# Kernel optimization log

Hardware: AMD Instinct MI355X
Metric: run time of the kernel (lower is better)

Reference implementation:

```python
import jax, jax.numpy as jnp
import numpy as np

FRAC_BIT = 12
SCALE = float(2 ** FRAC_BIT)          # 12 fractional bits
QMIN, QMAX = -32768.0, 32767.0        # signed 16-bit two's complement range


def quant16(x):
    """Quantize to signed 16-bit fixed point with 12 fractional bits.

    Matches float_to_16bits_tensor / bit_slice semantics: the bit-serial
    crossbar MVM of the sliced operands equals an exact integer product of
    these fixed-point values, rescaled back to float.
    """
    return jnp.clip(jnp.round(x * SCALE), QMIN, QMAX) / SCALE


def setup_inputs() -> dict:
    key = jax.random.key(0)
    k1, k2 = jax.random.split(key)
    x = jax.random.normal(k1, (32, 128, 56, 56), dtype=jnp.float32)
    # kaiming-ish scale so weights are well inside the fixed-point range
    weight = jax.random.normal(k2, (256, 128, 3, 3), dtype=jnp.float32) * 0.05
    return {"x": x, "weight": weight}


def reference(x, weight):
    # The nested i/j loop in the original slides a stride-1 window over the
    # zero-padded input, performing a bit-sliced crossbar MVM per pixel.
    # That is exactly conv2d(stride=1, padding=1) on 16-bit fixed-point
    # quantized input and weight (bias row in the crossbar is zero / unused).
    qx = quant16(x)
    qw = quant16(weight)
    out = jax.lax.conv_general_dilated(
        qx, qw,
        window_strides=(1, 1),
        padding=((1, 1), (1, 1)),
        dimension_numbers=("NCHW", "OIHW", "NCHW"),
    )
    return out
```

## Files before the change

### kernel.cpp

```cpp
#include <hip/hip_runtime.h>
#include <cstdint>
#include <cstddef>


typedef __attribute__((ext_vector_type(8))) short short8;
typedef __attribute__((ext_vector_type(4))) float floatx4;

#define NIMG 32
#define CIN  128
#define HW   56
#define KOUT 256
#define HP   58
#define XPAD_ELEMS ((size_t)NIMG * HP * HP * CIN)
#define WT_OFF_BYTES (XPAD_ELEMS * 2)
#define KK 1152

__device__ __forceinline__ uint16_t quant_bf16(float v) {
    float q = rintf(v * 4096.0f);
    q = fminf(fmaxf(q, -32768.0f), 32767.0f) * (1.0f / 4096.0f);
    union { float f; uint32_t u; } cv; cv.f = q;
    uint32_t u = cv.u;
    return (uint16_t)((u + 0x7fffu + ((u >> 16) & 1u)) >> 16);
}

__global__ __launch_bounds__(256) void quant_pad_x(const float* __restrict__ x,
                                                   uint16_t* __restrict__ xp) {
    const int b = blockIdx.x;
    const int n = b / HP, hp = b - n * HP;
    uint16_t* row = xp + (size_t)(n * HP + hp) * HP * CIN;

    if (hp == 0 || hp == HP - 1) {
        uint4 z{0, 0, 0, 0};
        uint4* d = (uint4*)row;
        for (int t = threadIdx.x; t < HP * CIN * 2 / 16; t += 256) d[t] = z;
        return;
    }
    const int h = hp - 1;
    __shared__ uint16_t tile[HW * 130];
    const float* src = x + (size_t)n * CIN * HW * HW + (size_t)h * HW;
    for (int t = threadIdx.x; t < CIN * 14; t += 256) {
        int c = t / 14, w4 = t - c * 14;
        float4 v = *(const float4*)(src + (size_t)c * (HW * HW) + w4 * 4);
        int base = (w4 * 4) * 130 + c;
        tile[base]       = quant_bf16(v.x);
        tile[base + 130] = quant_bf16(v.y);
        tile[base + 260] = quant_bf16(v.z);
        tile[base + 390] = quant_bf16(v.w);
    }
    __syncthreads();
    if (threadIdx.x < 32) {
        uint4 z{0, 0, 0, 0};
        if (threadIdx.x < 16) ((uint4*)row)[threadIdx.x] = z;
        else ((uint4*)(row + 57 * CIN))[threadIdx.x - 16] = z;
    }
    uint2* dst = (uint2*)(row + CIN);
    for (int t = threadIdx.x; t < (HW * CIN) / 4; t += 256) {
        int w = t >> 5, c4 = (t & 31) * 4;
        uint32_t a = tile[w * 130 + c4]     | ((uint32_t)tile[w * 130 + c4 + 1] << 16);
        uint32_t c = tile[w * 130 + c4 + 2] | ((uint32_t)tile[w * 130 + c4 + 3] << 16);
        dst[t] = make_uint2(a, c);
    }
}

__global__ __launch_bounds__(256) void quant_w(const float* __restrict__ w,
                                               uint16_t* __restrict__ wt) {
    int i = blockIdx.x * 256 + threadIdx.x;
    int k = i / KK;
    int r = i - k * KK;
    int tap = r >> 7;
    int c = r & 127;
    wt[i] = quant_bf16(w[(size_t)(k * CIN + c) * 9 + tap]);
}


#define GLOAD(gsrc, ldst)                                                      \
    __builtin_amdgcn_global_load_lds(                                          \
        (__attribute__((address_space(1))) void*)(void*)(gsrc),                \
        (__attribute__((address_space(3))) void*)(void*)(ldst), 16, 0, 0)

#define STAGE_A(bsel, kt) do {                                                 \
    GLOAD(aGp[0][0] + (size_t)(kt) * 64, &ldsA[bsel][0][(wv * 8) * 64]);       \
    GLOAD(aGp[0][1] + (size_t)(kt) * 64, &ldsA[bsel][0][(64 + wv * 8) * 64]);  \
    GLOAD(aGp[1][0] + (size_t)(kt) * 64, &ldsA[bsel][1][(wv * 8) * 64]);       \
    GLOAD(aGp[1][1] + (size_t)(kt) * 64, &ldsA[bsel][1][(64 + wv * 8) * 64]);  \
} while (0)

#define STAGE_B(bsel, kt) do {                                                 \
    const int tap_ = (kt) >> 1;                                                \
    const size_t boff_ = (size_t)((tap_ / 3) * HP + (tap_ % 3)) * CIN          \
                       + (size_t)((kt) & 1) * 64;                              \
    GLOAD(bGp[0][0] + boff_, &ldsB[bsel][0][(wv * 8) * 64]);                   \
    GLOAD(bGp[0][1] + boff_, &ldsB[bsel][0][(64 + wv * 8) * 64]);              \
    GLOAD(bGp[1][0] + boff_, &ldsB[bsel][1][(wv * 8) * 64]);                   \
    GLOAD(bGp[1][1] + boff_, &ldsB[bsel][1][(64 + wv * 8) * 64]);              \
} while (0)

#define READ_A(bsel, q4) do {                                                  \
    _Pragma("unroll")                                                          \
    for (int f_ = 0; f_ < 4; ++f_) {                                           \
        const int r_ = (q4) * 64 + f_ * 16 + m16;                              \
        ra[f_][0] = *(const short8*)&ldsA[bsel][wm][r_ * 64 + sl0];            \
        ra[f_][1] = *(const short8*)&ldsA[bsel][wm][r_ * 64 + sl1];            \
    }                                                                          \
} while (0)

#define READ_B(dst, bsel, ch) do {                                             \
    _Pragma("unroll")                                                          \
    for (int fc_ = 0; fc_ < 2; ++fc_) {                                        \
        const int r_ = bl + (ch) * 32 + fc_ * 16 + m16;                        \
        dst[fc_][0] = *(const short8*)&ldsB[bsel][bh][r_ * 64 + sl0];          \
        dst[fc_][1] = *(const short8*)&ldsB[bsel][bh][r_ * 64 + sl1];          \
    }                                                                          \
} while (0)

#define MFMA_Q(q4, ch, B) do {                                                 \
    _Pragma("unroll")                                                          \
    for (int s_ = 0; s_ < 2; ++s_)                                             \
    _Pragma("unroll")                                                          \
    for (int f_ = 0; f_ < 4; ++f_)                                             \
    _Pragma("unroll")                                                          \
    for (int c_ = 0; c_ < 2; ++c_)                                             \
        acc[q4][f_][ch][c_] = __builtin_amdgcn_mfma_f32_16x16x32_bf16(         \
            ra[f_][s_], B[c_][s_], acc[q4][f_][ch][c_], 0, 0, 0);              \
} while (0)

#define KT_BODY(bsel) do {                                                     \
    READ_A(bsel, 0);                                                           \
    READ_B(rb0, bsel, 0);                                                      \
    READ_B(rb1, bsel, 1);                                                      \
    __builtin_amdgcn_s_setprio(1);                                             \
    MFMA_Q(0, 0, rb0);                                                         \
    MFMA_Q(0, 1, rb1);                                                         \
    __builtin_amdgcn_s_setprio(0);                                             \
    READ_A(bsel, 1);                   \
    __builtin_amdgcn_s_setprio(1);                                             \
    MFMA_Q(1, 0, rb0);                                                         \
    MFMA_Q(1, 1, rb1);                                                         \
    __builtin_amdgcn_s_setprio(0);                                             \
} while (0)

#define KT_SYNC_STAGE(bsel, ktn) do {                                          \
    __builtin_amdgcn_s_barrier();                                              \
    STAGE_A(bsel, ktn); STAGE_B(bsel, ktn);                                    \
    asm volatile("s_waitcnt vmcnt(8)" ::: "memory");                           \
    __builtin_amdgcn_s_barrier();                                              \
} while (0)

__global__ __launch_bounds__(512, 2) void conv_gemm(const uint16_t* __restrict__ xp,
                                                    const uint16_t* __restrict__ wt,
                                                    float* __restrict__ out) {
    __shared__ __align__(16) uint16_t ldsA[2][2][128 * 64];
    __shared__ __align__(16) uint16_t ldsB[2][2][128 * 64];

    const int tid  = threadIdx.x;
    const int l    = tid & 63;
    const int wv   = tid >> 6;
    const int wm   = wv >> 2;
    const int wn   = wv & 3;
    const int bh   = wn >> 1;
    const int bl   = (wn & 1) * 64;
    const int srow = l >> 3;
    const int c_data = (l & 7) ^ srow;
    const int m16  = l & 15;
    const int q    = l >> 4;
    const int r7   = m16 & 7;
    const int sl0  = ((0 + q) ^ r7) * 8;
    const int sl1  = ((4 + q) ^ r7) * 8;

    const int b = blockIdx.x;
    const int pxblk = (b & 7) * 49 + (b >> 3);

    const uint16_t* aGp[2][2];
    const uint16_t* bGp[2][2];
#pragma unroll
    for (int h_ = 0; h_ < 2; ++h_)
#pragma unroll
        for (int j_ = 0; j_ < 2; ++j_) {
            const int row = h_ * 128 + j_ * 64 + wv * 8 + srow;
            aGp[h_][j_] = wt + (size_t)row * KK + c_data * 8;
            const int p = pxblk * 256 + row;
            const int n = p / 3136; const int rem = p - n * 3136;
            const int hh = rem / HW; const int ww = rem - hh * HW;
            bGp[h_][j_] = xp + (size_t)((n * HP + hh) * HP + ww) * CIN + c_data * 8;
        }

    floatx4 acc[2][4][2][2];
#pragma unroll
    for (int a_ = 0; a_ < 2; ++a_)
#pragma unroll
        for (int f_ = 0; f_ < 4; ++f_)
#pragma unroll
            for (int c_ = 0; c_ < 2; ++c_)
#pragma unroll
                for (int d_ = 0; d_ < 2; ++d_)
                    acc[a_][f_][c_][d_] = (floatx4){0.f, 0.f, 0.f, 0.f};

    short8 ra[4][2];
    short8 rb0[2][2];
    short8 rb1[2][2];

    STAGE_A(0, 0); STAGE_B(0, 0);
    STAGE_A(1, 1); STAGE_B(1, 1);
    asm volatile("s_waitcnt vmcnt(8)" ::: "memory");
    __builtin_amdgcn_s_barrier();

#pragma unroll 1
    for (int it = 0; it < 8; ++it) {
        const int ktE = 2 * it + 2;
        const int ktO = 2 * it + 3;
        KT_BODY(0);
        KT_SYNC_STAGE(0, ktE);
        KT_BODY(1);
        KT_SYNC_STAGE(1, ktO);
    }

    KT_BODY(0);
    __builtin_amdgcn_s_barrier();
    asm volatile("s_waitcnt vmcnt(0)" ::: "memory");
    __builtin_amdgcn_s_barrier();
    KT_BODY(1);

#pragma unroll
    for (int ch = 0; ch < 2; ++ch) {
        const int p0 = pxblk * 256 + wn * 64 + ch * 32 + m16;
        const int n = p0 / 3136; const int rem0 = p0 - n * 3136;
        float* opb = out + (size_t)(n * KOUT + wm * 128) * 3136 + rem0;
#pragma unroll
        for (int q4 = 0; q4 < 2; ++q4)
#pragma unroll
            for (int f = 0; f < 4; ++f) {
                const int kl = q4 * 64 + f * 16 + q * 4;
#pragma unroll
                for (int t = 0; t < 4; ++t) {
                    float* op = opb + (size_t)(kl + t) * 3136;
                    op[0]  = acc[q4][f][ch][0][t];
                    op[16] = acc[q4][f][ch][1][t];
                }
            }
    }
}

extern "C" void kernel_launch(void* const* d_in, const int* in_sizes, int n_in,
                              void* d_out, int out_size, void* d_ws, size_t ws_size,
                              hipStream_t stream) {
    const float* x = (const float*)d_in[0];
    const float* w = (const float*)d_in[1];
    float* out = (float*)d_out;

    uint16_t* xp  = (uint16_t*)d_ws;
    uint16_t* wtb = (uint16_t*)((char*)d_ws + WT_OFF_BYTES);

    quant_pad_x<<<NIMG * HP, 256, 0, stream>>>(x, xp);
    quant_w<<<(KOUT * KK) / 256, 256, 0, stream>>>(w, wtb);

    conv_gemm<<<dim3(392), dim3(512), 0, stream>>>(xp, wtb, out);
}
```

Baseline: 212.7 us.

## Load weight operand directly from global into registers, bypassing LDS staging

Removes the LDS buffers for the weight (A) tiles and has each lane read its A fragments straight from global memory (expected to be cache-resident) into registers. The q4=0 fragment for the next k-step is prefetched in the tail, and the q4=1 fragment is loaded mid-body. This halves LDS footprint and drops the A LDS writes and reads. In exchange, the global-load latency for A sits closer to the MFMA critical path, the per-row reads are only partly coalesced, and the counter-based waits now mix register loads with the asynchronous LDS loads, which may force tighter waits.

Result: slower. 301.8 us (+41.9%).

```diff
diff --git a/kernel.cpp b/kernel.cpp
--- a/kernel.cpp
+++ b/kernel.cpp
@@ -78,13 +78,6 @@
         (__attribute__((address_space(1))) void*)(void*)(gsrc),                \
         (__attribute__((address_space(3))) void*)(void*)(ldst), 16, 0, 0)
 
-#define STAGE_A(bsel, kt) do {                                                 \
-    GLOAD(aGp[0][0] + (size_t)(kt) * 64, &ldsA[bsel][0][(wv * 8) * 64]);       \
-    GLOAD(aGp[0][1] + (size_t)(kt) * 64, &ldsA[bsel][0][(64 + wv * 8) * 64]);  \
-    GLOAD(aGp[1][0] + (size_t)(kt) * 64, &ldsA[bsel][1][(wv * 8) * 64]);       \
-    GLOAD(aGp[1][1] + (size_t)(kt) * 64, &ldsA[bsel][1][(64 + wv * 8) * 64]);  \
-} while (0)
-
 #define STAGE_B(bsel, kt) do {                                                 \
     const int tap_ = (kt) >> 1;                                                \
     const size_t boff_ = (size_t)((tap_ / 3) * HP + (tap_ % 3)) * CIN          \
@@ -95,12 +88,12 @@
     GLOAD(bGp[1][1] + boff_, &ldsB[bsel][1][(64 + wv * 8) * 64]);              \
 } while (0)
 
-#define READ_A(bsel, q4) do {                                                  \
+#define LOAD_A(q4, kt) do {                                                    \
+    const uint16_t* ab_ = aB + (kt) * 64;                                      \
     _Pragma("unroll")                                                          \
     for (int f_ = 0; f_ < 4; ++f_) {                                           \
-        const int r_ = (q4) * 64 + f_ * 16 + m16;                              \
-        ra[f_][0] = *(const short8*)&ldsA[bsel][wm][r_ * 64 + sl0];            \
-        ra[f_][1] = *(const short8*)&ldsA[bsel][wm][r_ * 64 + sl1];            \
+        ra[f_][0] = *(const short8*)(ab_ + ((q4) * 64 + f_ * 16) * KK);        \
+        ra[f_][1] = *(const short8*)(ab_ + ((q4) * 64 + f_ * 16) * KK + 32);   \
     }                                                                          \
 } while (0)
 
@@ -124,32 +117,31 @@
             ra[f_][s_], B[c_][s_], acc[q4][f_][ch][c_], 0, 0, 0);              \
 } while (0)
 
-#define KT_BODY(bsel) do {                                                     \
-    READ_A(bsel, 0);                                                           \
+#define KT_BODY(bsel, kt) do {                                                 \
     READ_B(rb0, bsel, 0);                                                      \
     READ_B(rb1, bsel, 1);                                                      \
     __builtin_amdgcn_s_setprio(1);                                             \
     MFMA_Q(0, 0, rb0);                                                         \
     MFMA_Q(0, 1, rb1);                                                         \
     __builtin_amdgcn_s_setprio(0);                                             \
-    READ_A(bsel, 1);                   \
+    LOAD_A(1, kt);                    \
     __builtin_amdgcn_s_setprio(1);                                             \
     MFMA_Q(1, 0, rb0);                                                         \
     MFMA_Q(1, 1, rb1);                                                         \
     __builtin_amdgcn_s_setprio(0);                                             \
 } while (0)
 
-#define KT_SYNC_STAGE(bsel, ktn) do {                                          \
+#define KT_TAIL(bsel, ktp1, ktp2) do {                                         \
     __builtin_amdgcn_s_barrier();                                              \
-    STAGE_A(bsel, ktn); STAGE_B(bsel, ktn);                                    \
-    asm volatile("s_waitcnt vmcnt(8)" ::: "memory");                           \
+    LOAD_A(0, ktp1);                  \
+    STAGE_B(bsel, ktp2);              \
+    asm volatile("s_waitcnt vmcnt(12)" ::: "memory");                          \
     __builtin_amdgcn_s_barrier();                                              \
 } while (0)
 
 __global__ __launch_bounds__(512, 2) void conv_gemm(const uint16_t* __restrict__ xp,
                                                     const uint16_t* __restrict__ wt,
                                                     float* __restrict__ out) {
-    __shared__ __align__(16) uint16_t ldsA[2][2][128 * 64];
     __shared__ __align__(16) uint16_t ldsB[2][2][128 * 64];
 
     const int tid  = threadIdx.x;
@@ -170,14 +162,14 @@
     const int b = blockIdx.x;
     const int pxblk = (b & 7) * 49 + (b >> 3);
 
-    const uint16_t* aGp[2][2];
+    const uint16_t* aB = wt + (size_t)((wm * 128 + m16) * KK + q * 8);
+
     const uint16_t* bGp[2][2];
 #pragma unroll
     for (int h_ = 0; h_ < 2; ++h_)
 #pragma unroll
         for (int j_ = 0; j_ < 2; ++j_) {
             const int row = h_ * 128 + j_ * 64 + wv * 8 + srow;
-            aGp[h_][j_] = wt + (size_t)row * KK + c_data * 8;
             const int p = pxblk * 256 + row;
             const int n = p / 3136; const int rem = p - n * 3136;
             const int hh = rem / HW; const int ww = rem - hh * HW;
@@ -199,26 +191,27 @@
     short8 rb0[2][2];
     short8 rb1[2][2];
 
-    STAGE_A(0, 0); STAGE_B(0, 0);
-    STAGE_A(1, 1); STAGE_B(1, 1);
+    LOAD_A(0, 0);
+    STAGE_B(0, 0);
+    STAGE_B(1, 1);
+    asm volatile("s_waitcnt vmcnt(4)" ::: "memory");
+    __builtin_amdgcn_s_barrier();
+
+#pragma unroll 1
+    for (int it = 0; it < 8; ++it) {
+        const int kt0 = 2 * it;
+        KT_BODY(0, kt0);
+        KT_TAIL(0, kt0 + 1, kt0 + 2);
+        KT_BODY(1, kt0 + 1);
+        KT_TAIL(1, kt0 + 2, kt0 + 3);
+    }
+
+    KT_BODY(0, 16);
+    __builtin_amdgcn_s_barrier();
+    LOAD_A(0, 17);
     asm volatile("s_waitcnt vmcnt(8)" ::: "memory");
     __builtin_amdgcn_s_barrier();
-
-#pragma unroll 1
-    for (int it = 0; it < 8; ++it) {
-        const int ktE = 2 * it + 2;
-        const int ktO = 2 * it + 3;
-        KT_BODY(0);
-        KT_SYNC_STAGE(0, ktE);
-        KT_BODY(1);
-        KT_SYNC_STAGE(1, ktO);
-    }
-
-    KT_BODY(0);
-    __builtin_amdgcn_s_barrier();
-    asm volatile("s_waitcnt vmcnt(0)" ::: "memory");
-    __builtin_amdgcn_s_barrier();
-    KT_BODY(1);
+    KT_BODY(1, 17);
 
 #pragma unroll
     for (int ch = 0; ch < 2; ++ch) {
```

## Pre-tile weights per k-step and vectorize input transpose through shared memory

Applied to the files above, without the earlier changes.

The quantized weight buffer is reordered so that each 64-wide k-slice for all 256 output rows sits contiguously, which makes the GEMM's A-tile global-to-LDS loads walk a single contiguous 32KB block per k-step instead of strided rows of length 1152. The input quantize/pad kernel now quantizes four channels per thread and writes packed 8-byte chunks into a 136-padded LDS tile, then copies out 16-byte vectors, in place of scattered 2-byte shared stores. This targets memory access efficiency in both the preprocessing and the main loop, at the cost of four times the loads in flight per thread in the transpose.

Measured after the change: 208.6 us. Within noise of the previous version (-2.0%).

```diff
diff --git a/kernel.cpp b/kernel.cpp
--- a/kernel.cpp
+++ b/kernel.cpp
@@ -23,6 +23,11 @@
     return (uint16_t)((u + 0x7fffu + ((u >> 16) & 1u)) >> 16);
 }
 
+__device__ __forceinline__ float f4c(float4 v, int k) {
+    switch (k) { case 0: return v.x; case 1: return v.y;
+                 case 2: return v.z; default: return v.w; }
+}
+
 __global__ __launch_bounds__(256) void quant_pad_x(const float* __restrict__ x,
                                                    uint16_t* __restrict__ xp) {
     const int b = blockIdx.x;
@@ -36,16 +41,24 @@
         return;
     }
     const int h = hp - 1;
-    __shared__ uint16_t tile[HW * 130];
+    __shared__ __align__(16) uint16_t tile[HW * 136];
     const float* src = x + (size_t)n * CIN * HW * HW + (size_t)h * HW;
-    for (int t = threadIdx.x; t < CIN * 14; t += 256) {
-        int c = t / 14, w4 = t - c * 14;
-        float4 v = *(const float4*)(src + (size_t)c * (HW * HW) + w4 * 4);
-        int base = (w4 * 4) * 130 + c;
-        tile[base]       = quant_bf16(v.x);
-        tile[base + 130] = quant_bf16(v.y);
-        tile[base + 260] = quant_bf16(v.z);
-        tile[base + 390] = quant_bf16(v.w);
+    for (int t = threadIdx.x; t < 32 * 14; t += 256) {
+        int cg = t / 14, w4 = t - cg * 14;
+        int c4 = cg * 4;
+        float4 v0 = *(const float4*)(src + (size_t)(c4 + 0) * (HW * HW) + w4 * 4);
+        float4 v1 = *(const float4*)(src + (size_t)(c4 + 1) * (HW * HW) + w4 * 4);
+        float4 v2 = *(const float4*)(src + (size_t)(c4 + 2) * (HW * HW) + w4 * 4);
+        float4 v3 = *(const float4*)(src + (size_t)(c4 + 3) * (HW * HW) + w4 * 4);
+#pragma unroll
+        for (int k = 0; k < 4; ++k) {
+            int w = w4 * 4 + k;
+            uint32_t lo = (uint32_t)quant_bf16(f4c(v0, k)) |
+                          ((uint32_t)quant_bf16(f4c(v1, k)) << 16);
+            uint32_t hi = (uint32_t)quant_bf16(f4c(v2, k)) |
+                          ((uint32_t)quant_bf16(f4c(v3, k)) << 16);
+            *(uint2*)&tile[w * 136 + c4] = make_uint2(lo, hi);
+        }
     }
     __syncthreads();
     if (threadIdx.x < 32) {
@@ -53,23 +66,23 @@
         if (threadIdx.x < 16) ((uint4*)row)[threadIdx.x] = z;
         else ((uint4*)(row + 57 * CIN))[threadIdx.x - 16] = z;
     }
-    uint2* dst = (uint2*)(row + CIN);
-    for (int t = threadIdx.x; t < (HW * CIN) / 4; t += 256) {
-        int w = t >> 5, c4 = (t & 31) * 4;
-        uint32_t a = tile[w * 130 + c4]     | ((uint32_t)tile[w * 130 + c4 + 1] << 16);
-        uint32_t c = tile[w * 130 + c4 + 2] | ((uint32_t)tile[w * 130 + c4 + 3] << 16);
-        dst[t] = make_uint2(a, c);
+    uint4* dst = (uint4*)(row + CIN);
+    for (int t = threadIdx.x; t < HW * 16; t += 256) {
+        int w = t >> 4, c8 = (t & 15) * 8;
+        dst[t] = *(const uint4*)&tile[w * 136 + c8];
     }
 }
 
 __global__ __launch_bounds__(256) void quant_w(const float* __restrict__ w,
                                                uint16_t* __restrict__ wt) {
     int i = blockIdx.x * 256 + threadIdx.x;
-    int k = i / KK;
-    int r = i - k * KK;
-    int tap = r >> 7;
-    int c = r & 127;
-    wt[i] = quant_bf16(w[(size_t)(k * CIN + c) * 9 + tap]);
+    int kt = i >> 14;
+    int rem = i & 16383;
+    int r = rem >> 6;
+    int j = rem & 63;
+    int tap = kt >> 1;
+    int c = ((kt & 1) << 6) + j;
+    wt[i] = quant_bf16(w[(size_t)(r * CIN + c) * 9 + tap]);
 }
 
 
@@ -79,10 +92,11 @@
         (__attribute__((address_space(3))) void*)(void*)(ldst), 16, 0, 0)
 
 #define STAGE_A(bsel, kt) do {                                                 \
-    GLOAD(aGp[0][0] + (size_t)(kt) * 64, &ldsA[bsel][0][(wv * 8) * 64]);       \
-    GLOAD(aGp[0][1] + (size_t)(kt) * 64, &ldsA[bsel][0][(64 + wv * 8) * 64]);  \
-    GLOAD(aGp[1][0] + (size_t)(kt) * 64, &ldsA[bsel][1][(wv * 8) * 64]);       \
-    GLOAD(aGp[1][1] + (size_t)(kt) * 64, &ldsA[bsel][1][(64 + wv * 8) * 64]);  \
+    const uint16_t* as_ = wt + (size_t)(kt) * 16384 + a00;                     \
+    GLOAD(as_,         &ldsA[bsel][0][(wv * 8) * 64]);                         \
+    GLOAD(as_ + 4096,  &ldsA[bsel][0][(64 + wv * 8) * 64]);                    \
+    GLOAD(as_ + 8192,  &ldsA[bsel][1][(wv * 8) * 64]);                         \
+    GLOAD(as_ + 12288, &ldsA[bsel][1][(64 + wv * 8) * 64]);                    \
 } while (0)
 
 #define STAGE_B(bsel, kt) do {                                                 \
@@ -170,14 +184,14 @@
     const int b = blockIdx.x;
     const int pxblk = (b & 7) * 49 + (b >> 3);
 
-    const uint16_t* aGp[2][2];
+    const int a00 = (wv * 8 + srow) * 64 + c_data * 8;
+
     const uint16_t* bGp[2][2];
 #pragma unroll
     for (int h_ = 0; h_ < 2; ++h_)
 #pragma unroll
         for (int j_ = 0; j_ < 2; ++j_) {
             const int row = h_ * 128 + j_ * 64 + wv * 8 + srow;
-            aGp[h_][j_] = wt + (size_t)row * KK + c_data * 8;
             const int p = pxblk * 256 + row;
             const int n = p / 3136; const int rem = p - n * 3136;
             const int hh = rem / HW; const int ww = rem - hh * HW;
```
